# Kernel tuning notes

Measured on AMD Instinct MI355X. Metric: run time of the kernel, lower is better.

The kernel has to match this reference:

```python
import jax, jax.numpy as jnp
import numpy as np
from jax import lax

B, CIN, COUT, K, L = 128, 8, 64, 33, 4096
STRIDE, PAD = 1, 16
HID, NW = 128, 3  # agent hidden, num wavelet types (morlet, mexhat, laplace)
MEXHAT_NORM = 2.0 / (np.sqrt(3.0) * np.pi ** 0.25)


def setup_inputs() -> dict:
    key = jax.random.key(0)
    ks = jax.random.split(key, 12)
    s = 0.05  # small init scale for agent weights
    return {
        "x": jax.random.normal(ks[0], (B, CIN, L), jnp.float32),
        # torch init: ones; add small noise so per-wavelet scales differ
        "superparams": jnp.ones((COUT, CIN, NW), jnp.float32)
        + 0.1 * jax.random.normal(ks[1], (COUT, CIN, NW), jnp.float32),
        "threshold": jnp.full((COUT,), 0.1, jnp.float32),
        "fw": s * jax.random.normal(ks[2], (2 * CIN, HID), jnp.float32),
        "fb": jnp.zeros((HID,), jnp.float32),
        "vw1": s * jax.random.normal(ks[3], (HID, HID), jnp.float32),
        "vb1": jnp.zeros((HID,), jnp.float32),
        "vw2": s * jax.random.normal(ks[4], (HID, 1), jnp.float32),
        "vb2": jnp.zeros((1,), jnp.float32),
        "aw1": s * jax.random.normal(ks[5], (HID, HID), jnp.float32),
        "ab1": jnp.zeros((HID,), jnp.float32),
        "aw2": s * jax.random.normal(ks[6], (HID, NW), jnp.float32),
        "ab2": jnp.zeros((NW,), jnp.float32),
    }


def _softplus_pos(p):
    return jax.nn.softplus(p) + 1e-6


def _make_kernels(superparams):
    # superparams: [COUT, CIN, NW] -> kernel bank [NW, COUT, CIN, K]
    grid = jnp.arange(-(K // 2), K // 2 + 1, dtype=jnp.float32)  # [K]
    scale = _softplus_pos(superparams)  # [COUT, CIN, NW]
    kernels = []
    for i, name in enumerate(("morlet", "mexhat", "laplace")):
        xi = grid[None, None, :] / scale[:, :, i : i + 1]  # [COUT, CIN, K]
        if name == "morlet":
            ker = jnp.exp(-0.5 * xi * xi) * jnp.cos(5.0 * xi)
        elif name == "mexhat":
            ker = MEXHAT_NORM * (1.0 - xi * xi) * jnp.exp(-0.5 * xi * xi)
        else:  # laplace
            ker = jnp.sign(grid)[None, None, :] * jnp.exp(-jnp.abs(xi))
        ker = ker - ker.mean(axis=-1, keepdims=True)
        ker = ker / (jnp.linalg.norm(ker, axis=-1, keepdims=True) + 1e-6)
        kernels.append(ker)
    return jnp.stack(kernels, axis=0)  # [NW, COUT, CIN, K]


def _q_values(states, fw, fb, vw1, vb1, vw2, vb2, aw1, ab1, aw2, ab2):
    h = jax.nn.relu(states @ fw + fb)                     # [B, HID]
    v = jax.nn.relu(h @ vw1 + vb1) @ vw2 + vb2            # [B, 1]
    a = jax.nn.relu(h @ aw1 + ab1) @ aw2 + ab2            # [B, NW]
    return v + a - a.mean(axis=1, keepdims=True)


def reference(x, superparams, threshold, fw, fb, vw1, vb1, vw2, vb2,
              aw1, ab1, aw2, ab2):
    # RL state: per-channel mean & (unbiased) std of the signal -> [B, 2*CIN]
    states = jnp.concatenate([x.mean(axis=-1), x.std(axis=-1, ddof=1)], axis=1)
    q = _q_values(states, fw, fb, vw1, vb1, vw2, vb2, aw1, ab1, aw2, ab2)
    actions = jnp.argmax(q, axis=1)                        # [B], greedy (eval)

    kernels = _make_kernels(superparams)                   # [NW, COUT, CIN, K]
    w_sel = kernels[actions]                               # [B, COUT, CIN, K]

    def conv_one(xb, wb):  # xb [CIN, L], wb [COUT, CIN, K]
        return lax.conv_general_dilated(
            xb[None], wb, window_strides=(STRIDE,), padding=[(PAD, PAD)],
            dimension_numbers=("NCH", "OIH", "NCH"))[0]

    y = jax.vmap(conv_one)(x, w_sel)                       # [B, COUT, Lout]

    # soft shrinkage (denoising) with strictly positive learnable threshold
    tau = _softplus_pos(threshold)[None, :, None]
    return jnp.sign(y) * jnp.maximum(jnp.abs(y) - tau, 0.0)
```

## Files before the change

### kernel.cpp

```cpp
#include <hip/hip_runtime.h>
#include <hip/hip_bf16.h>
#include <cmath>

#define B     128
#define CIN   8
#define COUT  64
#define K     33
#define KP    36
#define KKD   (KP * CIN)
#define NSL   (KKD / 32)
#define L     4096
#define PAD   16
#define HID   128
#define NW    3

#define TL    512
#define NROW  (TL + KP)

typedef __attribute__((ext_vector_type(8))) short short8;
typedef __attribute__((ext_vector_type(4))) float f32x4;

__device__ __forceinline__ float softplusf(float v) {
    return (v > 20.f) ? v : log1pf(expf(v));
}

__global__ __launch_bounds__(256) void agent_kernel(
    const float* __restrict__ x,
    const float* __restrict__ fw, const float* __restrict__ fb,
    const float* __restrict__ aw1, const float* __restrict__ ab1,
    const float* __restrict__ aw2, const float* __restrict__ ab2,
    int* __restrict__ actions)
{
    const int b = blockIdx.x;
    const int tid = threadIdx.x;
    __shared__ float st[2 * CIN];
    __shared__ float h[HID];
    __shared__ float ha[HID];

    const int ci  = tid >> 5;
    const int sub = tid & 31;
    const float* xp = x + ((size_t)b * CIN + ci) * L;
    float s = 0.f, ss = 0.f;
    for (int j = sub; j < L / 4; j += 32) {
        float4 v = ((const float4*)xp)[j];
        s  += v.x + v.y + v.z + v.w;
        ss += v.x * v.x + v.y * v.y + v.z * v.z + v.w * v.w;
    }
    for (int m = 16; m; m >>= 1) {
        s  += __shfl_xor(s,  m);
        ss += __shfl_xor(ss, m);
    }
    if (sub == 0) {
        float mean = s / (float)L;
        float var  = fmaxf(ss - s * mean, 0.f) / (float)(L - 1);
        st[ci]       = mean;
        st[CIN + ci] = sqrtf(var);
    }
    __syncthreads();

    const int j = tid;
    if (j < HID) {
        float acc = fb[j];
        #pragma unroll
        for (int i = 0; i < 2 * CIN; ++i) acc = fmaf(st[i], fw[i * HID + j], acc);
        h[j] = fmaxf(acc, 0.f);
    }
    __syncthreads();
    if (j < HID) {
        float acc2 = ab1[j];
        for (int i = 0; i < HID; ++i) acc2 = fmaf(h[i], aw1[i * HID + j], acc2);
        ha[j] = fmaxf(acc2, 0.f);
    }
    __syncthreads();
    if (j == 0) {
        float best = -1e30f; int bi = 0;
        for (int w = 0; w < NW; ++w) {
            float a = ab2[w];
            for (int i = 0; i < HID; ++i) a = fmaf(ha[i], aw2[i * NW + w], a);
            if (a > best) { best = a; bi = w; }
        }
        actions[b] = bi;
    }
}

__global__ __launch_bounds__(256) void bank_kernel(
    const float* __restrict__ sp, __hip_bfloat16* __restrict__ bankbf)
{
    const int t = blockIdx.x * blockDim.x + threadIdx.x;
    if (t >= NW * COUT * CIN) return;
    const int nw = t >> 9;
    const int co = (t >> 3) & 63;
    const int ci = t & 7;

    const float p = sp[(co * CIN + ci) * NW + nw];
    const float scale = softplusf(p) + 1e-6f;

    float ker[K];
    float mean = 0.f;
    #pragma unroll
    for (int k = 0; k < K; ++k) {
        float g  = (float)(k - K / 2);
        float xi = g / scale;
        float v;
        if (nw == 0) {
            v = expf(-0.5f * xi * xi) * cosf(5.f * xi);
        } else if (nw == 1) {
            v = 0.8673250705840776f * (1.f - xi * xi) * expf(-0.5f * xi * xi);
        } else {
            float sgn = (g > 0.f) ? 1.f : ((g < 0.f) ? -1.f : 0.f);
            v = sgn * expf(-fabsf(xi));
        }
        ker[k] = v; mean += v;
    }
    mean *= (1.f / (float)K);
    float nrm = 0.f;
    #pragma unroll
    for (int k = 0; k < K; ++k) { ker[k] -= mean; nrm += ker[k] * ker[k]; }
    const float inv = 1.f / (sqrtf(nrm) + 1e-6f);

    __hip_bfloat16* dst = bankbf + ((size_t)(nw * COUT + co)) * KKD + ci;
    #pragma unroll
    for (int k = 0; k < K; ++k) dst[k * CIN] = __float2bfloat16(ker[k] * inv);
    #pragma unroll
    for (int k = K; k < KP; ++k) dst[k * CIN] = __float2bfloat16(0.f);
}

__global__ __launch_bounds__(256, 2) void conv_kernel(
    const float* __restrict__ x, const __hip_bfloat16* __restrict__ bankbf,
    const int* __restrict__ actions, const float* __restrict__ threshold,
    float* __restrict__ out)
{
    const int b  = blockIdx.y;
    const int l0 = blockIdx.x * TL;
    const int tid = threadIdx.x;
    const int lane = tid & 63;
    const int w    = tid >> 6;
    const int g    = lane >> 4;
    const int ln   = lane & 15;

    __shared__ short8 xT[NROW];

    {
        __hip_bfloat16* xb = (__hip_bfloat16*)xT;
        for (int idx = tid; idx < CIN * NROW; idx += 256) {
            int ci = idx / NROW;
            int r  = idx - ci * NROW;
            int gp = l0 - PAD + r;
            float f = (gp >= 0 && gp < L) ? x[((size_t)b * CIN + ci) * L + gp] : 0.f;
            xb[r * CIN + ci] = __float2bfloat16(f);
        }
    }

    const int act = __builtin_amdgcn_readfirstlane(actions[b]);
    const short8* wq = (const short8*)(bankbf + (size_t)act * COUT * KKD);
    short8 aQ[4][NSL];
    #pragma unroll
    for (int ct = 0; ct < 4; ++ct) {
        const short8* wrow = wq + (ct * 16 + ln) * (KKD / 8);
        #pragma unroll
        for (int s = 0; s < NSL; ++s) aQ[ct][s] = wrow[4 * s + g];
    }

    float tau[4][4];
    #pragma unroll
    for (int ct = 0; ct < 4; ++ct)
        #pragma unroll
        for (int jj = 0; jj < 4; ++jj)
            tau[ct][jj] = softplusf(threshold[ct * 16 + 4 * g + jj]) + 1e-6f;

    __syncthreads();

    const int wl0 = w * (TL / 4);
    for (int lt = 0; lt < (TL / 4) / 16; ++lt) {
        const int lbase = wl0 + lt * 16;
        const int row0  = lbase + ln + g;
        f32x4 acc[4] = {{0.f,0.f,0.f,0.f},{0.f,0.f,0.f,0.f},
                        {0.f,0.f,0.f,0.f},{0.f,0.f,0.f,0.f}};
        #pragma unroll
        for (int s = 0; s < NSL; ++s) {
            short8 bfrag = xT[row0 + 4 * s];
            acc[0] = __builtin_amdgcn_mfma_f32_16x16x32_bf16(aQ[0][s], bfrag, acc[0], 0, 0, 0);
            acc[1] = __builtin_amdgcn_mfma_f32_16x16x32_bf16(aQ[1][s], bfrag, acc[1], 0, 0, 0);
            acc[2] = __builtin_amdgcn_mfma_f32_16x16x32_bf16(aQ[2][s], bfrag, acc[2], 0, 0, 0);
            acc[3] = __builtin_amdgcn_mfma_f32_16x16x32_bf16(aQ[3][s], bfrag, acc[3], 0, 0, 0);
        }
        #pragma unroll
        for (int ct = 0; ct < 4; ++ct) {
            const int co = ct * 16 + 4 * g;
            #pragma unroll
            for (int jj = 0; jj < 4; ++jj) {
                float y = acc[ct][jj];
                float r = copysignf(fmaxf(fabsf(y) - tau[ct][jj], 0.f), y);
                out[((size_t)b * COUT + co + jj) * L + l0 + lbase + ln] = r;
            }
        }
    }
}

extern "C" void kernel_launch(void* const* d_in, const int* in_sizes, int n_in,
                              void* d_out, int out_size, void* d_ws, size_t ws_size,
                              hipStream_t stream)
{
    const float* x           = (const float*)d_in[0];
    const float* superparams = (const float*)d_in[1];
    const float* threshold   = (const float*)d_in[2];
    const float* fw          = (const float*)d_in[3];
    const float* fb          = (const float*)d_in[4];
    const float* aw1         = (const float*)d_in[9];
    const float* ab1         = (const float*)d_in[10];
    const float* aw2         = (const float*)d_in[11];
    const float* ab2         = (const float*)d_in[12];
    float* out = (float*)d_out;

    int* actions            = (int*)d_ws;
    __hip_bfloat16* bankbf  = (__hip_bfloat16*)((char*)d_ws + 1024);

    agent_kernel<<<B, 256, 0, stream>>>(x, fw, fb, aw1, ab1, aw2, ab2, actions);
    bank_kernel<<<(NW * COUT * CIN + 255) / 256, 256, 0, stream>>>(superparams, bankbf);
    conv_kernel<<<dim3(L / TL, B), 256, 0, stream>>>(x, bankbf, actions, threshold, out);
}
```

Before: 231.7 us.

## Merge agent and bank kernels; split conv output channels across 8 waves

```diff
diff --git a/kernel.cpp b/kernel.cpp
--- a/kernel.cpp
+++ b/kernel.cpp
@@ -24,117 +24,119 @@
     return (v > 20.f) ? v : log1pf(expf(v));
 }
 
-__global__ __launch_bounds__(256) void agent_kernel(
+__global__ __launch_bounds__(256) void prologue_kernel(
     const float* __restrict__ x,
     const float* __restrict__ fw, const float* __restrict__ fb,
     const float* __restrict__ aw1, const float* __restrict__ ab1,
     const float* __restrict__ aw2, const float* __restrict__ ab2,
-    int* __restrict__ actions)
+    const float* __restrict__ sp,
+    int* __restrict__ actions, __hip_bfloat16* __restrict__ bankbf)
 {
-    const int b = blockIdx.x;
     const int tid = threadIdx.x;
-    __shared__ float st[2 * CIN];
-    __shared__ float h[HID];
-    __shared__ float ha[HID];
-
-    const int ci  = tid >> 5;
-    const int sub = tid & 31;
-    const float* xp = x + ((size_t)b * CIN + ci) * L;
-    float s = 0.f, ss = 0.f;
-    for (int j = sub; j < L / 4; j += 32) {
-        float4 v = ((const float4*)xp)[j];
-        s  += v.x + v.y + v.z + v.w;
-        ss += v.x * v.x + v.y * v.y + v.z * v.z + v.w * v.w;
-    }
-    for (int m = 16; m; m >>= 1) {
-        s  += __shfl_xor(s,  m);
-        ss += __shfl_xor(ss, m);
-    }
-    if (sub == 0) {
-        float mean = s / (float)L;
-        float var  = fmaxf(ss - s * mean, 0.f) / (float)(L - 1);
-        st[ci]       = mean;
-        st[CIN + ci] = sqrtf(var);
-    }
-    __syncthreads();
-
-    const int j = tid;
-    if (j < HID) {
-        float acc = fb[j];
-        #pragma unroll
-        for (int i = 0; i < 2 * CIN; ++i) acc = fmaf(st[i], fw[i * HID + j], acc);
-        h[j] = fmaxf(acc, 0.f);
-    }
-    __syncthreads();
-    if (j < HID) {
-        float acc2 = ab1[j];
-        for (int i = 0; i < HID; ++i) acc2 = fmaf(h[i], aw1[i * HID + j], acc2);
-        ha[j] = fmaxf(acc2, 0.f);
-    }
-    __syncthreads();
-    if (j == 0) {
-        float best = -1e30f; int bi = 0;
-        for (int w = 0; w < NW; ++w) {
-            float a = ab2[w];
-            for (int i = 0; i < HID; ++i) a = fmaf(ha[i], aw2[i * NW + w], a);
-            if (a > best) { best = a; bi = w; }
-        }
-        actions[b] = bi;
-    }
-}
-
-__global__ __launch_bounds__(256) void bank_kernel(
-    const float* __restrict__ sp, __hip_bfloat16* __restrict__ bankbf)
-{
-    const int t = blockIdx.x * blockDim.x + threadIdx.x;
-    if (t >= NW * COUT * CIN) return;
-    const int nw = t >> 9;
-    const int co = (t >> 3) & 63;
-    const int ci = t & 7;
-
-    const float p = sp[(co * CIN + ci) * NW + nw];
-    const float scale = softplusf(p) + 1e-6f;
-
-    float ker[K];
-    float mean = 0.f;
-    #pragma unroll
-    for (int k = 0; k < K; ++k) {
-        float g  = (float)(k - K / 2);
-        float xi = g / scale;
-        float v;
-        if (nw == 0) {
-            v = expf(-0.5f * xi * xi) * cosf(5.f * xi);
-        } else if (nw == 1) {
-            v = 0.8673250705840776f * (1.f - xi * xi) * expf(-0.5f * xi * xi);
-        } else {
-            float sgn = (g > 0.f) ? 1.f : ((g < 0.f) ? -1.f : 0.f);
-            v = sgn * expf(-fabsf(xi));
-        }
-        ker[k] = v; mean += v;
-    }
-    mean *= (1.f / (float)K);
-    float nrm = 0.f;
-    #pragma unroll
-    for (int k = 0; k < K; ++k) { ker[k] -= mean; nrm += ker[k] * ker[k]; }
-    const float inv = 1.f / (sqrtf(nrm) + 1e-6f);
-
-    __hip_bfloat16* dst = bankbf + ((size_t)(nw * COUT + co)) * KKD + ci;
-    #pragma unroll
-    for (int k = 0; k < K; ++k) dst[k * CIN] = __float2bfloat16(ker[k] * inv);
-    #pragma unroll
-    for (int k = K; k < KP; ++k) dst[k * CIN] = __float2bfloat16(0.f);
-}
-
-__global__ __launch_bounds__(256, 2) void conv_kernel(
+
+    if (blockIdx.x < B) {
+        const int b = blockIdx.x;
+        __shared__ float st[2 * CIN];
+        __shared__ float h[HID];
+        __shared__ float ha[HID];
+
+        const int ci  = tid >> 5;
+        const int sub = tid & 31;
+        const float* xp = x + ((size_t)b * CIN + ci) * L;
+        float s = 0.f, ss = 0.f;
+        for (int j = sub; j < L / 4; j += 32) {
+            float4 v = ((const float4*)xp)[j];
+            s  += v.x + v.y + v.z + v.w;
+            ss += v.x * v.x + v.y * v.y + v.z * v.z + v.w * v.w;
+        }
+        for (int m = 16; m; m >>= 1) {
+            s  += __shfl_xor(s,  m);
+            ss += __shfl_xor(ss, m);
+        }
+        if (sub == 0) {
+            float mean = s / (float)L;
+            float var  = fmaxf(ss - s * mean, 0.f) / (float)(L - 1);
+            st[ci]       = mean;
+            st[CIN + ci] = sqrtf(var);
+        }
+        __syncthreads();
+
+        const int j = tid;
+        if (j < HID) {
+            float acc = fb[j];
+            #pragma unroll
+            for (int i = 0; i < 2 * CIN; ++i) acc = fmaf(st[i], fw[i * HID + j], acc);
+            h[j] = fmaxf(acc, 0.f);
+        }
+        __syncthreads();
+        if (j < HID) {
+            float acc2 = ab1[j];
+            for (int i = 0; i < HID; ++i) acc2 = fmaf(h[i], aw1[i * HID + j], acc2);
+            ha[j] = fmaxf(acc2, 0.f);
+        }
+        __syncthreads();
+        if (j == 0) {
+            float best = -1e30f; int bi = 0;
+            for (int w = 0; w < NW; ++w) {
+                float a = ab2[w];
+                for (int i = 0; i < HID; ++i) a = fmaf(ha[i], aw2[i * NW + w], a);
+                if (a > best) { best = a; bi = w; }
+            }
+            actions[b] = bi;
+        }
+    } else {
+        const int t = (blockIdx.x - B) * 256 + tid;
+        if (t >= NW * COUT * CIN) return;
+        const int nw = t >> 9;
+        const int co = (t >> 3) & 63;
+        const int ci = t & 7;
+
+        const float p = sp[(co * CIN + ci) * NW + nw];
+        const float scale = softplusf(p) + 1e-6f;
+
+        float ker[K];
+        float mean = 0.f;
+        #pragma unroll
+        for (int k = 0; k < K; ++k) {
+            float g  = (float)(k - K / 2);
+            float xi = g / scale;
+            float v;
+            if (nw == 0) {
+                v = expf(-0.5f * xi * xi) * cosf(5.f * xi);
+            } else if (nw == 1) {
+                v = 0.8673250705840776f * (1.f - xi * xi) * expf(-0.5f * xi * xi);
+            } else {
+                float sgn = (g > 0.f) ? 1.f : ((g < 0.f) ? -1.f : 0.f);
+                v = sgn * expf(-fabsf(xi));
+            }
+            ker[k] = v; mean += v;
+        }
+        mean *= (1.f / (float)K);
+        float nrm = 0.f;
+        #pragma unroll
+        for (int k = 0; k < K; ++k) { ker[k] -= mean; nrm += ker[k] * ker[k]; }
+        const float inv = 1.f / (sqrtf(nrm) + 1e-6f);
+
+        __hip_bfloat16* dst = bankbf + ((size_t)(nw * COUT + co)) * KKD + ci;
+        #pragma unroll
+        for (int k = 0; k < K; ++k) dst[k * CIN] = __float2bfloat16(ker[k] * inv);
+        #pragma unroll
+        for (int k = K; k < KP; ++k) dst[k * CIN] = __float2bfloat16(0.f);
+    }
+}
+
+__global__ __launch_bounds__(512, 4) void conv_kernel(
     const float* __restrict__ x, const __hip_bfloat16* __restrict__ bankbf,
     const int* __restrict__ actions, const float* __restrict__ threshold,
     float* __restrict__ out)
 {
     const int b  = blockIdx.y;
     const int l0 = blockIdx.x * TL;
-    const int tid = threadIdx.x;
+    const int tid  = threadIdx.x;
     const int lane = tid & 63;
     const int w    = tid >> 6;
+    const int p    = w & 1;
+    const int q    = w >> 1;
     const int g    = lane >> 4;
     const int ln   = lane & 15;
 
@@ -142,7 +144,7 @@
 
     {
         __hip_bfloat16* xb = (__hip_bfloat16*)xT;
-        for (int idx = tid; idx < CIN * NROW; idx += 256) {
+        for (int idx = tid; idx < CIN * NROW; idx += 512) {
             int ci = idx / NROW;
             int r  = idx - ci * NROW;
             int gp = l0 - PAD + r;
@@ -153,44 +155,41 @@
 
     const int act = __builtin_amdgcn_readfirstlane(actions[b]);
     const short8* wq = (const short8*)(bankbf + (size_t)act * COUT * KKD);
-    short8 aQ[4][NSL];
+    short8 aQ[2][NSL];
     #pragma unroll
-    for (int ct = 0; ct < 4; ++ct) {
-        const short8* wrow = wq + (ct * 16 + ln) * (KKD / 8);
-        #pragma unroll
-        for (int s = 0; s < NSL; ++s) aQ[ct][s] = wrow[4 * s + g];
-    }
-
-    float tau[4][4];
+    for (int cc = 0; cc < 2; ++cc) {
+        const short8* wrow = wq + ((2 * p + cc) * 16 + ln) * (KKD / 8);
+        #pragma unroll
+        for (int s = 0; s < NSL; ++s) aQ[cc][s] = wrow[4 * s + g];
+    }
+
+    float tau[2][4];
     #pragma unroll
-    for (int ct = 0; ct < 4; ++ct)
+    for (int cc = 0; cc < 2; ++cc)
         #pragma unroll
         for (int jj = 0; jj < 4; ++jj)
-            tau[ct][jj] = softplusf(threshold[ct * 16 + 4 * g + jj]) + 1e-6f;
+            tau[cc][jj] = softplusf(threshold[(2 * p + cc) * 16 + 4 * g + jj]) + 1e-6f;
 
     __syncthreads();
 
-    const int wl0 = w * (TL / 4);
+    const int wl0 = q * (TL / 4);
     for (int lt = 0; lt < (TL / 4) / 16; ++lt) {
         const int lbase = wl0 + lt * 16;
         const int row0  = lbase + ln + g;
-        f32x4 acc[4] = {{0.f,0.f,0.f,0.f},{0.f,0.f,0.f,0.f},
-                        {0.f,0.f,0.f,0.f},{0.f,0.f,0.f,0.f}};
+        f32x4 acc[2] = {{0.f,0.f,0.f,0.f},{0.f,0.f,0.f,0.f}};
         #pragma unroll
         for (int s = 0; s < NSL; ++s) {
             short8 bfrag = xT[row0 + 4 * s];
             acc[0] = __builtin_amdgcn_mfma_f32_16x16x32_bf16(aQ[0][s], bfrag, acc[0], 0, 0, 0);
             acc[1] = __builtin_amdgcn_mfma_f32_16x16x32_bf16(aQ[1][s], bfrag, acc[1], 0, 0, 0);
-            acc[2] = __builtin_amdgcn_mfma_f32_16x16x32_bf16(aQ[2][s], bfrag, acc[2], 0, 0, 0);
-            acc[3] = __builtin_amdgcn_mfma_f32_16x16x32_bf16(aQ[3][s], bfrag, acc[3], 0, 0, 0);
-        }
-        #pragma unroll
-        for (int ct = 0; ct < 4; ++ct) {
-            const int co = ct * 16 + 4 * g;
+        }
+        #pragma unroll
+        for (int cc = 0; cc < 2; ++cc) {
+            const int co = (2 * p + cc) * 16 + 4 * g;
             #pragma unroll
             for (int jj = 0; jj < 4; ++jj) {
-                float y = acc[ct][jj];
-                float r = copysignf(fmaxf(fabsf(y) - tau[ct][jj], 0.f), y);
+                float y = acc[cc][jj];
+                float r = copysignf(fmaxf(fabsf(y) - tau[cc][jj], 0.f), y);
                 out[((size_t)b * COUT + co + jj) * L + l0 + lbase + ln] = r;
             }
         }
@@ -215,7 +214,8 @@
     int* actions            = (int*)d_ws;
     __hip_bfloat16* bankbf  = (__hip_bfloat16*)((char*)d_ws + 1024);
 
-    agent_kernel<<<B, 256, 0, stream>>>(x, fw, fb, aw1, ab1, aw2, ab2, actions);
-    bank_kernel<<<(NW * COUT * CIN + 255) / 256, 256, 0, stream>>>(superparams, bankbf);
-    conv_kernel<<<dim3(L / TL, B), 256, 0, stream>>>(x, bankbf, actions, threshold, out);
-}
+    prologue_kernel<<<B + 6, 256, 0, stream>>>(
+        x, fw, fb, aw1, ab1, aw2, ab2, superparams, actions, bankbf);
+    conv_kernel<<<dim3(L / TL, B), 512, 0, stream>>>(
+        x, bankbf, actions, threshold, out);
+}
```

New measurement: 265.3 us. 14.5% more time.
